# Kernel optimization log

Hardware: AMD Instinct MI355X
Metric: run time of the kernel (lower is better)

Reference implementation:

```python
import jax, jax.numpy as jnp
import numpy as np

B, C, H, W = 8, 128, 64, 64

def conv2d(x, w, b, pad):
    # x: [B,C,H,W], w: [O,I,kh,kw] -> NCHW conv with symmetric padding
    y = jax.lax.conv_general_dilated(
        x, w, window_strides=(1, 1), padding=[(pad, pad), (pad, pad)],
        dimension_numbers=("NCHW", "OIHW", "NCHW"))
    return y + b[None, :, None, None]

def setup_inputs() -> dict:
    key = jax.random.key(0)
    ks = jax.random.split(key, 5)
    s3 = 1.0 / np.sqrt(C * 9)  # kaiming-uniform-ish scale for 3x3 conv
    s1 = 1.0 / np.sqrt(C)
    return {
        "x": jax.random.normal(ks[0], (B, C, H, W), jnp.float32),
        "Wq": jax.random.normal(ks[1], (C, C, 3, 3), jnp.float32) * s3,
        "bq": jnp.zeros((C,), jnp.float32),
        "Wk": jax.random.normal(ks[2], (C, C, 3, 3), jnp.float32) * s3,
        "bk": jnp.zeros((C,), jnp.float32),
        "Wv": jax.random.normal(ks[3], (C, C, 3, 3), jnp.float32) * s3,
        "bv": jnp.zeros((C,), jnp.float32),
        "Wo": jax.random.normal(ks[4], (C, C, 1, 1), jnp.float32) * s1,
        "bo": jnp.zeros((C,), jnp.float32),
    }

def reference(x, Wq, bq, Wk, bk, Wv, bv, Wo, bo):
    b, c, h, w = x.shape
    n = h * w
    scale = c ** (-0.5)
    # NOTE: original module defines self.norm but never applies it in forward.
    q = conv2d(x, Wq, bq, 1).reshape(b, c, n)
    k = conv2d(x, Wk, bk, 1).reshape(b, c, n)
    v = conv2d(x, Wv, bv, 1).reshape(b, c, n)
    attn = jax.nn.softmax(jnp.einsum("bci,bcj->bij", q, k) * scale, axis=2)  # [b,n,n]
    out = jnp.einsum("bij,bcj->bci", attn, v).reshape(b, c, h, w)
    out = conv2d(out, Wo, bo, 0)
    return x + out
```

## Files before the change

kernel.cpp:

```cpp
#include <hip/hip_runtime.h>

typedef __attribute__((ext_vector_type(8))) short bf16x8;
typedef __attribute__((ext_vector_type(4))) float f32x4;
typedef __attribute__((ext_vector_type(16))) float f32x16;

static __device__ __forceinline__ unsigned short f2bf(float f) {
    union { float f; unsigned int u; } v; v.f = f;
    unsigned int r = v.u + 0x7FFFu + ((v.u >> 16) & 1u);
    return (unsigned short)(r >> 16);
}

static __device__ __forceinline__ unsigned cvtpk_bf16(float lo, float hi) {
    unsigned r;
    asm("v_cvt_pk_bf16_f32 %0, %1, %2" : "=v"(r) : "v"(lo), "v"(hi));
    return r;
}

#define NRW (27 * 16384)

__global__ __launch_bounds__(256) void repack_k(const float* __restrict__ Wq, const float* __restrict__ Wk,
                                                const float* __restrict__ Wv, const float* __restrict__ Wo,
                                                unsigned short* __restrict__ RW, unsigned short* __restrict__ WoB) {
    int t = blockIdx.x * 256 + threadIdx.x;
    if (t < NRW) {
        int s = t & 7, o = (t >> 3) & 127, g = (t >> 10) & 3, cc = (t >> 12) & 3, tap = t >> 14;
        int conv = tap / 9, kk = tap % 9, kh = kk / 3, kw = kk % 3;
        int c = cc * 32 + g * 8 + s;
        const float* W = (conv == 0) ? Wq : ((conv == 1) ? Wk : Wv);
        RW[t] = f2bf(W[((o * 128 + c) * 3 + kh) * 3 + kw]);
    } else {
        int u = t - NRW;
        if (u < 16384) WoB[u] = f2bf(Wo[u]);
    }
}

__global__ __launch_bounds__(256) void qkv_conv_k(const float* __restrict__ x, const unsigned short* __restrict__ RW,
                                                  const float* __restrict__ bq, const float* __restrict__ bk,
                                                  const float* __restrict__ bv,
                                                  unsigned short* __restrict__ q_ws, unsigned short* __restrict__ k_ws,
                                                  unsigned short* __restrict__ v_ws) {
    __shared__ unsigned short xs[3 * 66 * 128];
    const int tid = threadIdx.x;
    const int b = blockIdx.x >> 6, h = blockIdx.x & 63;
    for (int i = tid; i < 3 * 66 * 128; i += 256) xs[i] = 0;
    __syncthreads();
    for (int ch = tid; ch < 3 * 128 * 16; ch += 256) {
        int r3 = ch >> 11, rem = ch & 2047, c = rem >> 4, w4 = rem & 15;
        int hh = h - 1 + r3;
        if (hh >= 0 && hh < 64) {
            float4 v = *(const float4*)(x + ((b * 128 + c) * 64 + hh) * 64 + w4 * 4);
            float vv[4] = {v.x, v.y, v.z, v.w};
#pragma unroll
            for (int j = 0; j < 4; ++j) {
                int wr = w4 * 4 + j + 1;
                unsigned int byte = (unsigned int)(((r3 * 66 + wr) * 128 + c) * 2) ^ ((wr & 7) << 4);
                *(unsigned short*)((char*)xs + byte) = f2bf(vv[j]);
            }
        }
    }
    __syncthreads();
    const int lane = tid & 63, wave = tid >> 6;
    const int l15 = lane & 15, g = lane >> 4;
    f32x4 acc[4][6];
#pragma unroll
    for (int i = 0; i < 4; ++i)
#pragma unroll
        for (int j = 0; j < 6; ++j) acc[i][j] = (f32x4){0.f, 0.f, 0.f, 0.f};
#pragma unroll 1
    for (int kk = 0; kk < 9; ++kk) {
        const int kw = kk % 3;
#pragma unroll 1
        for (int cc = 0; cc < 4; ++cc) {
            bf16x8 a[4];
#pragma unroll
            for (int mf = 0; mf < 4; ++mf) {
                int wr = mf * 16 + l15 + kw;
                unsigned int byte = (unsigned int)((((kk / 3) * 66 + wr) * 128 + cc * 32 + g * 8) * 2) ^ ((wr & 7) << 4);
                a[mf] = *(const bf16x8*)((const char*)xs + byte);
            }
#pragma unroll
            for (int n6 = 0; n6 < 6; ++n6) {
                int nt = wave * 6 + n6;
                int conv = nt >> 3;
                int o = (nt * 16 + l15) & 127;
                bf16x8 bfr = *(const bf16x8*)(RW + ((((conv * 9 + kk) * 4 + cc) * 4 + g) * 128 + o) * 8);
#pragma unroll
                for (int mf = 0; mf < 4; ++mf)
                    acc[mf][n6] = __builtin_amdgcn_mfma_f32_16x16x32_bf16(a[mf], bfr, acc[mf][n6], 0, 0, 0);
            }
        }
    }
    const float SCALE = 0.08838834764831845f;
#pragma unroll
    for (int n6 = 0; n6 < 6; ++n6) {
        int nt = wave * 6 + n6;
        int conv = nt >> 3;
        int o = (nt * 16 + l15) & 127;
        float bias = (conv == 0) ? bq[o] : ((conv == 1) ? bk[o] : bv[o]);
#pragma unroll
        for (int mf = 0; mf < 4; ++mf) {
#pragma unroll
            for (int r = 0; r < 4; ++r) {
                int pos = h * 64 + mf * 16 + g * 4 + r;
                float val = acc[mf][n6][r] + bias;
                if (conv == 0)      q_ws[(b * 4096 + pos) * 128 + o] = f2bf(val * SCALE);
                else if (conv == 1) k_ws[(b * 4096 + pos) * 128 + o] = f2bf(val);
                else                v_ws[(b * 128 + o) * 4096 + pos] = f2bf(val);
            }
        }
    }
}

#define AS1C(p) ((const __attribute__((address_space(1))) void*)(p))
#define AS3(p)  ((__attribute__((address_space(3))) void*)(p))

__global__ __launch_bounds__(512, 2) void attn_k(
    const unsigned short* __restrict__ q_ws, const unsigned short* __restrict__ k_ws,
    const unsigned short* __restrict__ v_ws, const unsigned short* __restrict__ WoB,
    const float* __restrict__ bo, const float* __restrict__ x, float* __restrict__ out) {
    __shared__ __align__(16) char smem[133120];

    const int tid = threadIdx.x;
    const int lane = tid & 63, wave = tid >> 6;
    const int wj = wave & 1, wi = wave >> 1;
    const int l31 = lane & 31, h = lane >> 5;
    const int b = blockIdx.x & 7;
    const int ibase = (blockIdx.x >> 3) * 128;
    const int irow = wi * 32 + l31;

    const char* kg[4]; const char* vg[4]; int ldsoff[4];
#pragma unroll
    for (int q = 0; q < 4; ++q) {
        int slot = (wave * 4 + q) * 64 + lane;
        int row = slot >> 4, s = slot & 15;
        int cs = s ^ (row & 15);
        kg[q] = (const char*)(k_ws + ((size_t)b * 4096 + row) * 128 + cs * 8);
        vg[q] = (const char*)(v_ws + ((size_t)b * 128 + row) * 4096 + cs * 8);
        ldsoff[q] = (wave * 4 + q) * 1024;
    }
#pragma unroll
    for (int q = 0; q < 4; ++q)
        __builtin_amdgcn_global_load_lds(AS1C(kg[q]), AS3(smem + ldsoff[q]), 16, 0, 0);
#pragma unroll
    for (int q = 0; q < 4; ++q)
        __builtin_amdgcn_global_load_lds(AS1C(vg[q]), AS3(smem + 32768 + ldsoff[q]), 16, 0, 0);

    bf16x8 qf[8];
    {
        const unsigned short* qrow = q_ws + ((size_t)b * 4096 + ibase + irow) * 128;
#pragma unroll
        for (int cc = 0; cc < 8; ++cc) qf[cc] = *(const bf16x8*)(qrow + cc * 16 + h * 8);
    }

    f32x16 oac[4];
#pragma unroll
    for (int cf = 0; cf < 4; ++cf)
#pragma unroll
        for (int r = 0; r < 16; ++r) oac[cf][r] = 0.f;
    float m = -1e30f, ssum = 0.f;

    __syncthreads();

#pragma unroll 1
    for (int kt = 0; kt < 32; ++kt) {
        const int cur = kt & 1;
        const char* Kc = smem + cur * 65536;
        const char* Vc = Kc + 32768;
        if (kt < 31) {
            char* Kn = smem + (cur ^ 1) * 65536;
            char* Vn = Kn + 32768;
            const size_t kb = (size_t)(kt + 1) * 32768;
            const size_t vb = (size_t)(kt + 1) * 256;
#pragma unroll
            for (int q = 0; q < 4; ++q)
                __builtin_amdgcn_global_load_lds(AS1C(kg[q] + kb), AS3(Kn + ldsoff[q]), 16, 0, 0);
#pragma unroll
            for (int q = 0; q < 4; ++q)
                __builtin_amdgcn_global_load_lds(AS1C(vg[q] + vb), AS3(Vn + ldsoff[q]), 16, 0, 0);
        }

        f32x16 st[2];
#pragma unroll
        for (int jf = 0; jf < 2; ++jf)
#pragma unroll
            for (int r = 0; r < 16; ++r) st[jf][r] = 0.f;
#pragma unroll
        for (int jf = 0; jf < 2; ++jf) {
            const int jrow = wj * 64 + jf * 32 + l31;
#pragma unroll
            for (int cc = 0; cc < 8; ++cc) {
                unsigned byte = (unsigned)(jrow * 256 + cc * 32 + h * 16) ^ ((jrow & 15) << 4);
                bf16x8 kf = *(const bf16x8*)(Kc + byte);
                st[jf] = __builtin_amdgcn_mfma_f32_32x32x16_bf16(kf, qf[cc], st[jf], 0, 0, 0);
            }
        }

        float tmax = -1e30f;
#pragma unroll
        for (int jf = 0; jf < 2; ++jf)
#pragma unroll
            for (int r = 0; r < 16; ++r) tmax = fmaxf(tmax, st[jf][r]);
        tmax = fmaxf(tmax, __shfl_xor(tmax, 32));
        if (!__all(tmax <= m)) {
            float mnew = fmaxf(m, tmax);
            float corr = __expf(m - mnew);
            ssum *= corr;
#pragma unroll
            for (int cf = 0; cf < 4; ++cf)
#pragma unroll
                for (int r = 0; r < 16; ++r) oac[cf][r] *= corr;
            m = mnew;
        }
        float psum = 0.f;
        unsigned u[2][4][2];
#pragma unroll
        for (int jf = 0; jf < 2; ++jf)
#pragma unroll
            for (int gq = 0; gq < 4; ++gq) {
                float p0 = __expf(st[jf][gq * 4 + 0] - m);
                float p1 = __expf(st[jf][gq * 4 + 1] - m);
                float p2 = __expf(st[jf][gq * 4 + 2] - m);
                float p3 = __expf(st[jf][gq * 4 + 3] - m);
                psum += (p0 + p1) + (p2 + p3);
                u[jf][gq][0] = cvtpk_bf16(p0, p1);
                u[jf][gq][1] = cvtpk_bf16(p2, p3);
            }
        psum += __shfl_xor(psum, 32);
        ssum += psum;

        bf16x8 pa[4];
#pragma unroll
        for (int js = 0; js < 4; ++js) {
            const int jf = js >> 1, ga = 2 * (js & 1), gb = ga + 1;
            unsigned own0 = h ? u[jf][gb][0] : u[jf][ga][0];
            unsigned own1 = h ? u[jf][gb][1] : u[jf][ga][1];
            unsigned snd0 = h ? u[jf][ga][0] : u[jf][gb][0];
            unsigned snd1 = h ? u[jf][ga][1] : u[jf][gb][1];
            unsigned rcv0 = __shfl_xor(snd0, 32);
            unsigned rcv1 = __shfl_xor(snd1, 32);
            union { unsigned w[4]; bf16x8 v; } pu;
            pu.w[0] = h ? rcv0 : own0;
            pu.w[1] = h ? rcv1 : own1;
            pu.w[2] = h ? own0 : rcv0;
            pu.w[3] = h ? own1 : rcv1;
            pa[js] = pu.v;
        }

#pragma unroll
        for (int js = 0; js < 4; ++js) {
            const int jcol = wj * 64 + js * 16 + h * 8;
#pragma unroll
            for (int cf = 0; cf < 4; ++cf) {
                int crow = cf * 32 + l31;
                unsigned vbyte = (unsigned)(crow * 256 + jcol * 2) ^ ((crow & 15) << 4);
                bf16x8 va = *(const bf16x8*)(Vc + vbyte);
                oac[cf] = __builtin_amdgcn_mfma_f32_32x32x16_bf16(va, pa[js], oac[cf], 0, 0, 0);
            }
        }
        __syncthreads();
    }

    float* sRed = (float*)(smem + 131072);
    if (h == 0) {
        sRed[(wave * 32 + l31) * 2] = m;
        sRed[(wave * 32 + l31) * 2 + 1] = ssum;
    }
    __syncthreads();
    float m1 = sRed[((wave ^ 1) * 32 + l31) * 2];
    float s1 = sRed[((wave ^ 1) * 32 + l31) * 2 + 1];
    float M = fmaxf(m, m1);
    float aS = __expf(m - M);
    float stot = aS * ssum + __expf(m1 - M) * s1;
    float inv = 1.0f / stot;

    float* sBig = (float*)smem;
    if (wj == 1) {
#pragma unroll
        for (int cf = 0; cf < 4; ++cf)
#pragma unroll
            for (int gq = 0; gq < 4; ++gq) {
                f32x4 v4;
#pragma unroll
                for (int k = 0; k < 4; ++k) v4[k] = aS * oac[cf][gq * 4 + k];
                int cb = cf * 32 + gq * 8 + 4 * h;
                unsigned byte = (unsigned)(wi * 16384 + l31 * 512 + cb * 4) ^ ((l31 & 7) << 4);
                *(f32x4*)((char*)sBig + byte) = v4;
            }
    }
    __syncthreads();
    unsigned short* sOut = (unsigned short*)(smem + 65536);
    if (wj == 0) {
#pragma unroll
        for (int cf = 0; cf < 4; ++cf)
#pragma unroll
            for (int gq = 0; gq < 4; ++gq) {
                int cb = cf * 32 + gq * 8 + 4 * h;
                unsigned rbyte = (unsigned)(wi * 16384 + l31 * 512 + cb * 4) ^ ((l31 & 7) << 4);
                f32x4 o4 = *(const f32x4*)((const char*)sBig + rbyte);
                float t0 = (aS * oac[cf][gq * 4 + 0] + o4[0]) * inv;
                float t1 = (aS * oac[cf][gq * 4 + 1] + o4[1]) * inv;
                float t2 = (aS * oac[cf][gq * 4 + 2] + o4[2]) * inv;
                float t3 = (aS * oac[cf][gq * 4 + 3] + o4[3]) * inv;
                uint2 pk;
                pk.x = cvtpk_bf16(t0, t1);
                pk.y = cvtpk_bf16(t2, t3);
                unsigned wbyte = (unsigned)(irow * 256 + cb * 2) ^ ((irow & 15) << 4);
                *(uint2*)((char*)sOut + wbyte) = pk;
            }
    }
    __syncthreads();

#pragma unroll
    for (int t = 0; t < 2; ++t) {
        int tt = wave + t * 8;
        int of = tt >> 2, ifl = tt & 3;
        int ir = ifl * 32 + l31;
        f32x16 acc;
#pragma unroll
        for (int r = 0; r < 16; ++r) acc[r] = 0.f;
#pragma unroll
        for (int cc = 0; cc < 8; ++cc) {
            unsigned bbyte = (unsigned)(ir * 256 + cc * 32 + h * 16) ^ ((ir & 15) << 4);
            bf16x8 bfr = *(const bf16x8*)((const char*)sOut + bbyte);
            bf16x8 wa = *(const bf16x8*)(WoB + (of * 32 + l31) * 128 + cc * 16 + h * 8);
            acc = __builtin_amdgcn_mfma_f32_32x32x16_bf16(wa, bfr, acc, 0, 0, 0);
        }
        int iglob = ibase + ir;
#pragma unroll
        for (int r = 0; r < 16; ++r) {
            int o = of * 32 + (r & 3) + 8 * (r >> 2) + 4 * h;
            size_t gidx = ((size_t)b * 128 + o) * 4096 + iglob;
            out[gidx] = acc[r] + bo[o] + x[gidx];
        }
    }
}

extern "C" void kernel_launch(void* const* d_in, const int* in_sizes, int n_in,
                              void* d_out, int out_size, void* d_ws, size_t ws_size,
                              hipStream_t stream) {
    const float* x  = (const float*)d_in[0];
    const float* Wq = (const float*)d_in[1];
    const float* bq = (const float*)d_in[2];
    const float* Wk = (const float*)d_in[3];
    const float* bk = (const float*)d_in[4];
    const float* Wv = (const float*)d_in[5];
    const float* bv = (const float*)d_in[6];
    const float* Wo = (const float*)d_in[7];
    const float* bo = (const float*)d_in[8];
    char* ws = (char*)d_ws;
    unsigned short* q_ws = (unsigned short*)(ws);
    unsigned short* k_ws = (unsigned short*)(ws + 8388608);
    unsigned short* v_ws = (unsigned short*)(ws + 16777216);
    unsigned short* RW   = (unsigned short*)(ws + 25165824);
    unsigned short* WoB  = (unsigned short*)(ws + 26050560);
    float* out = (float*)d_out;

    hipLaunchKernelGGL(repack_k, dim3(1792), dim3(256), 0, stream, Wq, Wk, Wv, Wo, RW, WoB);
    hipLaunchKernelGGL(qkv_conv_k, dim3(512), dim3(256), 0, stream, x, RW, bq, bk, bv, q_ws, k_ws, v_ws);
    hipLaunchKernelGGL(attn_k, dim3(256), dim3(512), 0, stream, q_ws, k_ws, v_ws, WoB, bo, x, out);
}
```

Before: 151.4 us.

## Split attention waves 2x4 so each K fragment feeds two query tiles

The attention kernel's wave layout changes from 4 query groups by 2 key splits to 2 query groups by 4 key splits. Each wave now holds two 32-row query tiles, so every K and V fragment read from LDS is reused across two MFMAs, halving LDS read traffic per MFMA. The P transpose now uses permlane32_swap instead of shuffles, and the final merge of the four partial softmax states takes an extra LDS reduction step. Accumulator registers double, which risks spills or lower occupancy. The conv kernel's inner channel loop is also unrolled by two.

```diff
diff --git a/kernel.cpp b/kernel.cpp
--- a/kernel.cpp
+++ b/kernel.cpp
@@ -69,7 +69,7 @@
 #pragma unroll 1
     for (int kk = 0; kk < 9; ++kk) {
         const int kw = kk % 3;
-#pragma unroll 1
+#pragma unroll 2
         for (int cc = 0; cc < 4; ++cc) {
             bf16x8 a[4];
 #pragma unroll
@@ -118,15 +118,14 @@
     const unsigned short* __restrict__ q_ws, const unsigned short* __restrict__ k_ws,
     const unsigned short* __restrict__ v_ws, const unsigned short* __restrict__ WoB,
     const float* __restrict__ bo, const float* __restrict__ x, float* __restrict__ out) {
-    __shared__ __align__(16) char smem[133120];
+    __shared__ __align__(16) char smem[135168];
 
     const int tid = threadIdx.x;
     const int lane = tid & 63, wave = tid >> 6;
-    const int wj = wave & 1, wi = wave >> 1;
+    const int wj = wave & 3, wi = wave >> 2;
     const int l31 = lane & 31, h = lane >> 5;
     const int b = blockIdx.x & 7;
     const int ibase = (blockIdx.x >> 3) * 128;
-    const int irow = wi * 32 + l31;
 
     const char* kg[4]; const char* vg[4]; int ldsoff[4];
 #pragma unroll
@@ -145,19 +144,22 @@
     for (int q = 0; q < 4; ++q)
         __builtin_amdgcn_global_load_lds(AS1C(vg[q]), AS3(smem + 32768 + ldsoff[q]), 16, 0, 0);
 
-    bf16x8 qf[8];
-    {
-        const unsigned short* qrow = q_ws + ((size_t)b * 4096 + ibase + irow) * 128;
-#pragma unroll
-        for (int cc = 0; cc < 8; ++cc) qf[cc] = *(const bf16x8*)(qrow + cc * 16 + h * 8);
-    }
-
-    f32x16 oac[4];
+    bf16x8 qf[2][8];
+#pragma unroll
+    for (int iq = 0; iq < 2; ++iq) {
+        const unsigned short* qrow = q_ws + ((size_t)b * 4096 + ibase + wi * 64 + iq * 32 + l31) * 128;
+#pragma unroll
+        for (int cc = 0; cc < 8; ++cc) qf[iq][cc] = *(const bf16x8*)(qrow + cc * 16 + h * 8);
+    }
+
+    f32x16 oac[4][2];
 #pragma unroll
     for (int cf = 0; cf < 4; ++cf)
 #pragma unroll
-        for (int r = 0; r < 16; ++r) oac[cf][r] = 0.f;
-    float m = -1e30f, ssum = 0.f;
+        for (int iq = 0; iq < 2; ++iq)
+#pragma unroll
+            for (int r = 0; r < 16; ++r) oac[cf][iq][r] = 0.f;
+    float m[2] = {-1e30f, -1e30f}, ssum[2] = {0.f, 0.f};
 
     __syncthreads();
 
@@ -181,80 +183,85 @@
 
         f32x16 st[2];
 #pragma unroll
-        for (int jf = 0; jf < 2; ++jf)
-#pragma unroll
-            for (int r = 0; r < 16; ++r) st[jf][r] = 0.f;
-#pragma unroll
-        for (int jf = 0; jf < 2; ++jf) {
-            const int jrow = wj * 64 + jf * 32 + l31;
-#pragma unroll
-            for (int cc = 0; cc < 8; ++cc) {
-                unsigned byte = (unsigned)(jrow * 256 + cc * 32 + h * 16) ^ ((jrow & 15) << 4);
-                bf16x8 kf = *(const bf16x8*)(Kc + byte);
-                st[jf] = __builtin_amdgcn_mfma_f32_32x32x16_bf16(kf, qf[cc], st[jf], 0, 0, 0);
-            }
-        }
-
-        float tmax = -1e30f;
-#pragma unroll
-        for (int jf = 0; jf < 2; ++jf)
-#pragma unroll
-            for (int r = 0; r < 16; ++r) tmax = fmaxf(tmax, st[jf][r]);
-        tmax = fmaxf(tmax, __shfl_xor(tmax, 32));
-        if (!__all(tmax <= m)) {
-            float mnew = fmaxf(m, tmax);
-            float corr = __expf(m - mnew);
-            ssum *= corr;
-#pragma unroll
-            for (int cf = 0; cf < 4; ++cf)
-#pragma unroll
-                for (int r = 0; r < 16; ++r) oac[cf][r] *= corr;
-            m = mnew;
-        }
-        float psum = 0.f;
+        for (int iq = 0; iq < 2; ++iq)
+#pragma unroll
+            for (int r = 0; r < 16; ++r) st[iq][r] = 0.f;
+        const int jrow = wj * 32 + l31;
+#pragma unroll
+        for (int cc = 0; cc < 8; ++cc) {
+            unsigned byte = (unsigned)(jrow * 256 + cc * 32 + h * 16) ^ ((jrow & 15) << 4);
+            bf16x8 kf = *(const bf16x8*)(Kc + byte);
+            st[0] = __builtin_amdgcn_mfma_f32_32x32x16_bf16(kf, qf[0][cc], st[0], 0, 0, 0);
+            st[1] = __builtin_amdgcn_mfma_f32_32x32x16_bf16(kf, qf[1][cc], st[1], 0, 0, 0);
+        }
+
+        float tm[2];
+#pragma unroll
+        for (int iq = 0; iq < 2; ++iq) {
+            float tmax = st[iq][0];
+#pragma unroll
+            for (int r = 1; r < 16; ++r) tmax = fmaxf(tmax, st[iq][r]);
+            tmax = fmaxf(tmax, __shfl_xor(tmax, 32));
+            tm[iq] = tmax;
+        }
+        if (!__all(tm[0] <= m[0] && tm[1] <= m[1])) {
+#pragma unroll
+            for (int iq = 0; iq < 2; ++iq) {
+                float mnew = fmaxf(m[iq], tm[iq]);
+                float corr = __expf(m[iq] - mnew);
+                ssum[iq] *= corr;
+#pragma unroll
+                for (int cf = 0; cf < 4; ++cf)
+#pragma unroll
+                    for (int r = 0; r < 16; ++r) oac[cf][iq][r] *= corr;
+                m[iq] = mnew;
+            }
+        }
         unsigned u[2][4][2];
 #pragma unroll
-        for (int jf = 0; jf < 2; ++jf)
+        for (int iq = 0; iq < 2; ++iq) {
+            float psum = 0.f;
 #pragma unroll
             for (int gq = 0; gq < 4; ++gq) {
-                float p0 = __expf(st[jf][gq * 4 + 0] - m);
-                float p1 = __expf(st[jf][gq * 4 + 1] - m);
-                float p2 = __expf(st[jf][gq * 4 + 2] - m);
-                float p3 = __expf(st[jf][gq * 4 + 3] - m);
+                float p0 = __expf(st[iq][gq * 4 + 0] - m[iq]);
+                float p1 = __expf(st[iq][gq * 4 + 1] - m[iq]);
+                float p2 = __expf(st[iq][gq * 4 + 2] - m[iq]);
+                float p3 = __expf(st[iq][gq * 4 + 3] - m[iq]);
                 psum += (p0 + p1) + (p2 + p3);
-                u[jf][gq][0] = cvtpk_bf16(p0, p1);
-                u[jf][gq][1] = cvtpk_bf16(p2, p3);
-            }
-        psum += __shfl_xor(psum, 32);
-        ssum += psum;
-
-        bf16x8 pa[4];
-#pragma unroll
-        for (int js = 0; js < 4; ++js) {
-            const int jf = js >> 1, ga = 2 * (js & 1), gb = ga + 1;
-            unsigned own0 = h ? u[jf][gb][0] : u[jf][ga][0];
-            unsigned own1 = h ? u[jf][gb][1] : u[jf][ga][1];
-            unsigned snd0 = h ? u[jf][ga][0] : u[jf][gb][0];
-            unsigned snd1 = h ? u[jf][ga][1] : u[jf][gb][1];
-            unsigned rcv0 = __shfl_xor(snd0, 32);
-            unsigned rcv1 = __shfl_xor(snd1, 32);
-            union { unsigned w[4]; bf16x8 v; } pu;
-            pu.w[0] = h ? rcv0 : own0;
-            pu.w[1] = h ? rcv1 : own1;
-            pu.w[2] = h ? own0 : rcv0;
-            pu.w[3] = h ? own1 : rcv1;
-            pa[js] = pu.v;
-        }
-
-#pragma unroll
-        for (int js = 0; js < 4; ++js) {
-            const int jcol = wj * 64 + js * 16 + h * 8;
+                u[iq][gq][0] = cvtpk_bf16(p0, p1);
+                u[iq][gq][1] = cvtpk_bf16(p2, p3);
+            }
+            psum += __shfl_xor(psum, 32);
+            ssum[iq] += psum;
+        }
+
+        bf16x8 pa[2][2];
+#pragma unroll
+        for (int js = 0; js < 2; ++js)
+#pragma unroll
+            for (int iq = 0; iq < 2; ++iq) {
+                unsigned a0 = u[iq][2 * js][0], b0 = u[iq][2 * js + 1][0];
+                unsigned a1 = u[iq][2 * js][1], b1 = u[iq][2 * js + 1][1];
+                auto r0 = __builtin_amdgcn_permlane32_swap(a0, b0, false, false);
+                auto r1 = __builtin_amdgcn_permlane32_swap(a1, b1, false, false);
+                union { unsigned w[4]; bf16x8 v; } pu;
+                pu.w[0] = r0[0];
+                pu.w[1] = r1[0];
+                pu.w[2] = r0[1];
+                pu.w[3] = r1[1];
+                pa[js][iq] = pu.v;
+            }
+
+#pragma unroll
+        for (int js = 0; js < 2; ++js) {
+            const int jcol = wj * 32 + js * 16 + h * 8;
 #pragma unroll
             for (int cf = 0; cf < 4; ++cf) {
                 int crow = cf * 32 + l31;
                 unsigned vbyte = (unsigned)(crow * 256 + jcol * 2) ^ ((crow & 15) << 4);
                 bf16x8 va = *(const bf16x8*)(Vc + vbyte);
-                oac[cf] = __builtin_amdgcn_mfma_f32_32x32x16_bf16(va, pa[js], oac[cf], 0, 0, 0);
+                oac[cf][0] = __builtin_amdgcn_mfma_f32_32x32x16_bf16(va, pa[js][0], oac[cf][0], 0, 0, 0);
+                oac[cf][1] = __builtin_amdgcn_mfma_f32_32x32x16_bf16(va, pa[js][1], oac[cf][1], 0, 0, 0);
             }
         }
         __syncthreads();
@@ -262,51 +269,101 @@
 
     float* sRed = (float*)(smem + 131072);
     if (h == 0) {
-        sRed[(wave * 32 + l31) * 2] = m;
-        sRed[(wave * 32 + l31) * 2 + 1] = ssum;
-    }
-    __syncthreads();
-    float m1 = sRed[((wave ^ 1) * 32 + l31) * 2];
-    float s1 = sRed[((wave ^ 1) * 32 + l31) * 2 + 1];
-    float M = fmaxf(m, m1);
-    float aS = __expf(m - M);
-    float stot = aS * ssum + __expf(m1 - M) * s1;
-    float inv = 1.0f / stot;
-
-    float* sBig = (float*)smem;
-    if (wj == 1) {
+#pragma unroll
+        for (int iq = 0; iq < 2; ++iq) {
+            int it = wi * 64 + iq * 32 + l31;
+            sRed[(wj * 128 + it) * 2] = m[iq];
+            sRed[(wj * 128 + it) * 2 + 1] = ssum[iq];
+        }
+    }
+    __syncthreads();
+    float aS[2];
+#pragma unroll
+    for (int iq = 0; iq < 2; ++iq) {
+        int it = wi * 64 + iq * 32 + l31;
+        float m0 = sRed[(0 * 128 + it) * 2], s0 = sRed[(0 * 128 + it) * 2 + 1];
+        float m1 = sRed[(1 * 128 + it) * 2], s1 = sRed[(1 * 128 + it) * 2 + 1];
+        float m2 = sRed[(2 * 128 + it) * 2], s2 = sRed[(2 * 128 + it) * 2 + 1];
+        float m3 = sRed[(3 * 128 + it) * 2], s3 = sRed[(3 * 128 + it) * 2 + 1];
+        float M = fmaxf(fmaxf(m0, m1), fmaxf(m2, m3));
+        float stot = __expf(m0 - M) * s0 + __expf(m1 - M) * s1 + __expf(m2 - M) * s2 + __expf(m3 - M) * s3;
+        aS[iq] = __expf(m[iq] - M) / stot;
+    }
+
+    float* sBig0 = (float*)smem;
+    float* sBig1 = (float*)(smem + 65536);
+    if (wj >= 2) {
+        char* B = (wj == 2) ? (char*)sBig0 : (char*)sBig1;
 #pragma unroll
         for (int cf = 0; cf < 4; ++cf)
 #pragma unroll
-            for (int gq = 0; gq < 4; ++gq) {
-                f32x4 v4;
-#pragma unroll
-                for (int k = 0; k < 4; ++k) v4[k] = aS * oac[cf][gq * 4 + k];
-                int cb = cf * 32 + gq * 8 + 4 * h;
-                unsigned byte = (unsigned)(wi * 16384 + l31 * 512 + cb * 4) ^ ((l31 & 7) << 4);
-                *(f32x4*)((char*)sBig + byte) = v4;
-            }
-    }
-    __syncthreads();
-    unsigned short* sOut = (unsigned short*)(smem + 65536);
+            for (int iq = 0; iq < 2; ++iq)
+#pragma unroll
+                for (int g = 0; g < 4; ++g) {
+                    int it = wi * 64 + iq * 32 + l31;
+                    int c = cf * 32 + g * 8 + 4 * h;
+                    f32x4 v;
+#pragma unroll
+                    for (int k = 0; k < 4; ++k) v[k] = oac[cf][iq][4 * g + k] * aS[iq];
+                    unsigned byte = (unsigned)(it * 512 + c * 4) ^ ((it & 7) << 4);
+                    *(f32x4*)(B + byte) = v;
+                }
+    }
+    __syncthreads();
     if (wj == 0) {
 #pragma unroll
         for (int cf = 0; cf < 4; ++cf)
 #pragma unroll
-            for (int gq = 0; gq < 4; ++gq) {
-                int cb = cf * 32 + gq * 8 + 4 * h;
-                unsigned rbyte = (unsigned)(wi * 16384 + l31 * 512 + cb * 4) ^ ((l31 & 7) << 4);
-                f32x4 o4 = *(const f32x4*)((const char*)sBig + rbyte);
-                float t0 = (aS * oac[cf][gq * 4 + 0] + o4[0]) * inv;
-                float t1 = (aS * oac[cf][gq * 4 + 1] + o4[1]) * inv;
-                float t2 = (aS * oac[cf][gq * 4 + 2] + o4[2]) * inv;
-                float t3 = (aS * oac[cf][gq * 4 + 3] + o4[3]) * inv;
-                uint2 pk;
-                pk.x = cvtpk_bf16(t0, t1);
-                pk.y = cvtpk_bf16(t2, t3);
-                unsigned wbyte = (unsigned)(irow * 256 + cb * 2) ^ ((irow & 15) << 4);
-                *(uint2*)((char*)sOut + wbyte) = pk;
-            }
+            for (int iq = 0; iq < 2; ++iq)
+#pragma unroll
+                for (int g = 0; g < 4; ++g) {
+                    int it = wi * 64 + iq * 32 + l31;
+                    int c = cf * 32 + g * 8 + 4 * h;
+                    unsigned byte = (unsigned)(it * 512 + c * 4) ^ ((it & 7) << 4);
+                    f32x4 rd = *(const f32x4*)((const char*)sBig0 + byte);
+#pragma unroll
+                    for (int k = 0; k < 4; ++k) oac[cf][iq][4 * g + k] = oac[cf][iq][4 * g + k] * aS[iq] + rd[k];
+                }
+    } else if (wj == 1) {
+#pragma unroll
+        for (int cf = 0; cf < 4; ++cf)
+#pragma unroll
+            for (int iq = 0; iq < 2; ++iq)
+#pragma unroll
+                for (int g = 0; g < 4; ++g) {
+                    int it = wi * 64 + iq * 32 + l31;
+                    int c = cf * 32 + g * 8 + 4 * h;
+                    unsigned byte = (unsigned)(it * 512 + c * 4) ^ ((it & 7) << 4);
+                    f32x4 rd = *(const f32x4*)((const char*)sBig1 + byte);
+                    f32x4 v;
+#pragma unroll
+                    for (int k = 0; k < 4; ++k) v[k] = oac[cf][iq][4 * g + k] * aS[iq] + rd[k];
+                    *(f32x4*)((char*)sBig1 + byte) = v;
+                }
+    }
+    __syncthreads();
+    unsigned short* sOut = (unsigned short*)smem;
+    if (wj == 0) {
+#pragma unroll
+        for (int cf = 0; cf < 4; ++cf)
+#pragma unroll
+            for (int iq = 0; iq < 2; ++iq)
+#pragma unroll
+                for (int g = 0; g < 4; ++g) {
+                    int it = wi * 64 + iq * 32 + l31;
+                    int c = cf * 32 + g * 8 + 4 * h;
+                    unsigned rbyte = (unsigned)(it * 512 + c * 4) ^ ((it & 7) << 4);
+                    f32x4 r1 = *(const f32x4*)((const char*)sBig1 + rbyte);
+                    float t0 = oac[cf][iq][4 * g + 0] + r1[0];
+                    float t1 = oac[cf][iq][4 * g + 1] + r1[1];
+                    float t2 = oac[cf][iq][4 * g + 2] + r1[2];
+                    float t3 = oac[cf][iq][4 * g + 3] + r1[3];
+                    uint2 pk;
+                    pk.x = cvtpk_bf16(t0, t1);
+                    pk.y = cvtpk_bf16(t2, t3);
+                    unsigned wbyte = (unsigned)(it * 256 + c * 2) ^ ((it & 15) << 4);
+                    *(uint2*)((char*)sOut + wbyte) = pk;
+                }
     }
     __syncthreads();
 
```

Result: slower. 280.0 us (+84.9%).

## Shrink attention tiles to 64 queries and 64 keys, doubling grid

Applied to the files above, without the earlier changes.

The attention kernel now uses 256-thread blocks that each handle 64 query rows, streaming 64-key K/V tiles (previously 128 and 128) with a smaller LDS footprint. The grid doubles to 512 blocks so more CUs stay busy. It also swaps the cross-half P exchange from shuffles to permlane32_swap, adds s_setprio around the MFMA sections, and unrolls the conv channel loop by two. In exchange there are twice as many loop iterations and barriers, K/V traffic per query rises, and each wave holds a smaller score tile.

```diff
diff --git a/kernel.cpp b/kernel.cpp
--- a/kernel.cpp
+++ b/kernel.cpp
@@ -69,7 +69,7 @@
 #pragma unroll 1
     for (int kk = 0; kk < 9; ++kk) {
         const int kw = kk % 3;
-#pragma unroll 1
+#pragma unroll 2
         for (int cc = 0; cc < 4; ++cc) {
             bf16x8 a[4];
 #pragma unroll
@@ -114,40 +114,45 @@
 #define AS1C(p) ((const __attribute__((address_space(1))) void*)(p))
 #define AS3(p)  ((__attribute__((address_space(3))) void*)(p))
 
-__global__ __launch_bounds__(512, 2) void attn_k(
+__global__ __launch_bounds__(256, 2) void attn_k(
     const unsigned short* __restrict__ q_ws, const unsigned short* __restrict__ k_ws,
     const unsigned short* __restrict__ v_ws, const unsigned short* __restrict__ WoB,
     const float* __restrict__ bo, const float* __restrict__ x, float* __restrict__ out) {
-    __shared__ __align__(16) char smem[133120];
+    __shared__ __align__(16) char smem[66560];
 
     const int tid = threadIdx.x;
     const int lane = tid & 63, wave = tid >> 6;
     const int wj = wave & 1, wi = wave >> 1;
     const int l31 = lane & 31, h = lane >> 5;
     const int b = blockIdx.x & 7;
-    const int ibase = (blockIdx.x >> 3) * 128;
-    const int irow = wi * 32 + l31;
-
-    const char* kg[4]; const char* vg[4]; int ldsoff[4];
-#pragma unroll
-    for (int q = 0; q < 4; ++q) {
-        int slot = (wave * 4 + q) * 64 + lane;
-        int row = slot >> 4, s = slot & 15;
-        int cs = s ^ (row & 15);
-        kg[q] = (const char*)(k_ws + ((size_t)b * 4096 + row) * 128 + cs * 8);
-        vg[q] = (const char*)(v_ws + ((size_t)b * 128 + row) * 4096 + cs * 8);
-        ldsoff[q] = (wave * 4 + q) * 1024;
-    }
-#pragma unroll
-    for (int q = 0; q < 4; ++q)
-        __builtin_amdgcn_global_load_lds(AS1C(kg[q]), AS3(smem + ldsoff[q]), 16, 0, 0);
-#pragma unroll
-    for (int q = 0; q < 4; ++q)
-        __builtin_amdgcn_global_load_lds(AS1C(vg[q]), AS3(smem + 32768 + ldsoff[q]), 16, 0, 0);
+    const int qt = blockIdx.x >> 3;
+    const int ibase = qt * 64;
+
+    const char* kB = (const char*)(k_ws + (size_t)b * 4096 * 128);
+    const char* vB = (const char*)(v_ws + (size_t)b * 128 * 4096);
+
+    auto stage = [&](int buf, int kt) {
+        char* Kn = smem + buf * 32768;
+        char* Vn = Kn + 16384;
+#pragma unroll
+        for (int q = 0; q < 4; ++q) {
+            int slot = (wave * 4 + q) * 64 + lane;
+            int krow = slot >> 4, ks = slot & 15;
+            int kcs = ks ^ (krow & 15);
+            __builtin_amdgcn_global_load_lds(AS1C(kB + (size_t)(kt * 64 + krow) * 256 + kcs * 16),
+                                             AS3(Kn + slot * 16), 16, 0, 0);
+            int vrow = slot >> 3, vs = slot & 7;
+            int vcs = vs ^ (vrow & 7);
+            __builtin_amdgcn_global_load_lds(AS1C(vB + (size_t)vrow * 8192 + kt * 128 + vcs * 16),
+                                             AS3(Vn + slot * 16), 16, 0, 0);
+        }
+    };
+
+    stage(0, 0);
 
     bf16x8 qf[8];
     {
-        const unsigned short* qrow = q_ws + ((size_t)b * 4096 + ibase + irow) * 128;
+        const unsigned short* qrow = q_ws + ((size_t)b * 4096 + ibase + wi * 32 + l31) * 128;
 #pragma unroll
         for (int cc = 0; cc < 8; ++cc) qf[cc] = *(const bf16x8*)(qrow + cc * 16 + h * 8);
     }
@@ -162,44 +167,28 @@
     __syncthreads();
 
 #pragma unroll 1
-    for (int kt = 0; kt < 32; ++kt) {
+    for (int kt = 0; kt < 64; ++kt) {
         const int cur = kt & 1;
-        const char* Kc = smem + cur * 65536;
-        const char* Vc = Kc + 32768;
-        if (kt < 31) {
-            char* Kn = smem + (cur ^ 1) * 65536;
-            char* Vn = Kn + 32768;
-            const size_t kb = (size_t)(kt + 1) * 32768;
-            const size_t vb = (size_t)(kt + 1) * 256;
-#pragma unroll
-            for (int q = 0; q < 4; ++q)
-                __builtin_amdgcn_global_load_lds(AS1C(kg[q] + kb), AS3(Kn + ldsoff[q]), 16, 0, 0);
-#pragma unroll
-            for (int q = 0; q < 4; ++q)
-                __builtin_amdgcn_global_load_lds(AS1C(vg[q] + vb), AS3(Vn + ldsoff[q]), 16, 0, 0);
-        }
-
-        f32x16 st[2];
-#pragma unroll
-        for (int jf = 0; jf < 2; ++jf)
-#pragma unroll
-            for (int r = 0; r < 16; ++r) st[jf][r] = 0.f;
-#pragma unroll
-        for (int jf = 0; jf < 2; ++jf) {
-            const int jrow = wj * 64 + jf * 32 + l31;
-#pragma unroll
-            for (int cc = 0; cc < 8; ++cc) {
-                unsigned byte = (unsigned)(jrow * 256 + cc * 32 + h * 16) ^ ((jrow & 15) << 4);
-                bf16x8 kf = *(const bf16x8*)(Kc + byte);
-                st[jf] = __builtin_amdgcn_mfma_f32_32x32x16_bf16(kf, qf[cc], st[jf], 0, 0, 0);
-            }
-        }
-
-        float tmax = -1e30f;
-#pragma unroll
-        for (int jf = 0; jf < 2; ++jf)
-#pragma unroll
-            for (int r = 0; r < 16; ++r) tmax = fmaxf(tmax, st[jf][r]);
+        const char* Kc = smem + cur * 32768;
+        const char* Vc = Kc + 16384;
+        if (kt < 63) stage(cur ^ 1, kt + 1);
+
+        f32x16 st;
+#pragma unroll
+        for (int r = 0; r < 16; ++r) st[r] = 0.f;
+        const int jrow = wj * 32 + l31;
+        __builtin_amdgcn_s_setprio(1);
+#pragma unroll
+        for (int cc = 0; cc < 8; ++cc) {
+            unsigned byte = (unsigned)(jrow * 256 + (((cc * 2 + h) ^ (jrow & 15)) << 4));
+            bf16x8 kf = *(const bf16x8*)(Kc + byte);
+            st = __builtin_amdgcn_mfma_f32_32x32x16_bf16(kf, qf[cc], st, 0, 0, 0);
+        }
+        __builtin_amdgcn_s_setprio(0);
+
+        float tmax = st[0];
+#pragma unroll
+        for (int r = 1; r < 16; ++r) tmax = fmaxf(tmax, st[r]);
         tmax = fmaxf(tmax, __shfl_xor(tmax, 32));
         if (!__all(tmax <= m)) {
             float mnew = fmaxf(m, tmax);
@@ -211,100 +200,95 @@
                 for (int r = 0; r < 16; ++r) oac[cf][r] *= corr;
             m = mnew;
         }
-        float psum = 0.f;
-        unsigned u[2][4][2];
-#pragma unroll
-        for (int jf = 0; jf < 2; ++jf)
-#pragma unroll
-            for (int gq = 0; gq < 4; ++gq) {
-                float p0 = __expf(st[jf][gq * 4 + 0] - m);
-                float p1 = __expf(st[jf][gq * 4 + 1] - m);
-                float p2 = __expf(st[jf][gq * 4 + 2] - m);
-                float p3 = __expf(st[jf][gq * 4 + 3] - m);
-                psum += (p0 + p1) + (p2 + p3);
-                u[jf][gq][0] = cvtpk_bf16(p0, p1);
-                u[jf][gq][1] = cvtpk_bf16(p2, p3);
-            }
-        psum += __shfl_xor(psum, 32);
-        ssum += psum;
-
-        bf16x8 pa[4];
-#pragma unroll
-        for (int js = 0; js < 4; ++js) {
-            const int jf = js >> 1, ga = 2 * (js & 1), gb = ga + 1;
-            unsigned own0 = h ? u[jf][gb][0] : u[jf][ga][0];
-            unsigned own1 = h ? u[jf][gb][1] : u[jf][ga][1];
-            unsigned snd0 = h ? u[jf][ga][0] : u[jf][gb][0];
-            unsigned snd1 = h ? u[jf][ga][1] : u[jf][gb][1];
-            unsigned rcv0 = __shfl_xor(snd0, 32);
-            unsigned rcv1 = __shfl_xor(snd1, 32);
+
+        float ps = 0.f;
+        bf16x8 pa[2];
+#pragma unroll
+        for (int js = 0; js < 2; ++js) {
+            float pA0 = __expf(st[8 * js + 0] - m);
+            float pA1 = __expf(st[8 * js + 1] - m);
+            float pA2 = __expf(st[8 * js + 2] - m);
+            float pA3 = __expf(st[8 * js + 3] - m);
+            float pB0 = __expf(st[8 * js + 4] - m);
+            float pB1 = __expf(st[8 * js + 5] - m);
+            float pB2 = __expf(st[8 * js + 6] - m);
+            float pB3 = __expf(st[8 * js + 7] - m);
+            ps += ((pA0 + pA1) + (pA2 + pA3)) + ((pB0 + pB1) + (pB2 + pB3));
+            unsigned a0 = cvtpk_bf16(pA0, pA1), a1 = cvtpk_bf16(pA2, pA3);
+            unsigned b0 = cvtpk_bf16(pB0, pB1), b1 = cvtpk_bf16(pB2, pB3);
+            auto r0 = __builtin_amdgcn_permlane32_swap(a0, b0, false, false);
+            auto r1 = __builtin_amdgcn_permlane32_swap(a1, b1, false, false);
             union { unsigned w[4]; bf16x8 v; } pu;
-            pu.w[0] = h ? rcv0 : own0;
-            pu.w[1] = h ? rcv1 : own1;
-            pu.w[2] = h ? own0 : rcv0;
-            pu.w[3] = h ? own1 : rcv1;
+            pu.w[0] = r0[0];
+            pu.w[1] = r1[0];
+            pu.w[2] = r0[1];
+            pu.w[3] = r1[1];
             pa[js] = pu.v;
         }
-
-#pragma unroll
-        for (int js = 0; js < 4; ++js) {
-            const int jcol = wj * 64 + js * 16 + h * 8;
+        ps += __shfl_xor(ps, 32);
+        ssum += ps;
+
+        __builtin_amdgcn_s_setprio(1);
+#pragma unroll
+        for (int js = 0; js < 2; ++js) {
+            const int chunk = wj * 4 + js * 2 + h;
 #pragma unroll
             for (int cf = 0; cf < 4; ++cf) {
                 int crow = cf * 32 + l31;
-                unsigned vbyte = (unsigned)(crow * 256 + jcol * 2) ^ ((crow & 15) << 4);
+                unsigned vbyte = (unsigned)(crow * 128 + ((chunk ^ (crow & 7)) << 4));
                 bf16x8 va = *(const bf16x8*)(Vc + vbyte);
                 oac[cf] = __builtin_amdgcn_mfma_f32_32x32x16_bf16(va, pa[js], oac[cf], 0, 0, 0);
             }
         }
+        __builtin_amdgcn_s_setprio(0);
         __syncthreads();
     }
 
-    float* sRed = (float*)(smem + 131072);
+    float* sRed = (float*)(smem + 65536);
+    const int it = wi * 32 + l31;
     if (h == 0) {
-        sRed[(wave * 32 + l31) * 2] = m;
-        sRed[(wave * 32 + l31) * 2 + 1] = ssum;
-    }
-    __syncthreads();
-    float m1 = sRed[((wave ^ 1) * 32 + l31) * 2];
-    float s1 = sRed[((wave ^ 1) * 32 + l31) * 2 + 1];
+        sRed[(wj * 64 + it) * 2] = m;
+        sRed[(wj * 64 + it) * 2 + 1] = ssum;
+    }
+    __syncthreads();
+    float m1 = sRed[((wj ^ 1) * 64 + it) * 2];
+    float s1 = sRed[((wj ^ 1) * 64 + it) * 2 + 1];
     float M = fmaxf(m, m1);
     float aS = __expf(m - M);
-    float stot = aS * ssum + __expf(m1 - M) * s1;
-    float inv = 1.0f / stot;
-
-    float* sBig = (float*)smem;
+    float inv = 1.0f / (aS * ssum + __expf(m1 - M) * s1);
+
+    char* sBig = smem + 32768;
     if (wj == 1) {
 #pragma unroll
         for (int cf = 0; cf < 4; ++cf)
 #pragma unroll
-            for (int gq = 0; gq < 4; ++gq) {
+            for (int g = 0; g < 4; ++g) {
+                int c = cf * 32 + g * 8 + 4 * h;
                 f32x4 v4;
 #pragma unroll
-                for (int k = 0; k < 4; ++k) v4[k] = aS * oac[cf][gq * 4 + k];
-                int cb = cf * 32 + gq * 8 + 4 * h;
-                unsigned byte = (unsigned)(wi * 16384 + l31 * 512 + cb * 4) ^ ((l31 & 7) << 4);
-                *(f32x4*)((char*)sBig + byte) = v4;
-            }
-    }
-    __syncthreads();
-    unsigned short* sOut = (unsigned short*)(smem + 65536);
+                for (int k = 0; k < 4; ++k) v4[k] = aS * oac[cf][4 * g + k];
+                unsigned byte = (unsigned)(it * 512 + c * 4) ^ ((it & 7) << 4);
+                *(f32x4*)(sBig + byte) = v4;
+            }
+    }
+    __syncthreads();
+    unsigned short* sOut = (unsigned short*)smem;
     if (wj == 0) {
 #pragma unroll
         for (int cf = 0; cf < 4; ++cf)
 #pragma unroll
-            for (int gq = 0; gq < 4; ++gq) {
-                int cb = cf * 32 + gq * 8 + 4 * h;
-                unsigned rbyte = (unsigned)(wi * 16384 + l31 * 512 + cb * 4) ^ ((l31 & 7) << 4);
-                f32x4 o4 = *(const f32x4*)((const char*)sBig + rbyte);
-                float t0 = (aS * oac[cf][gq * 4 + 0] + o4[0]) * inv;
-                float t1 = (aS * oac[cf][gq * 4 + 1] + o4[1]) * inv;
-                float t2 = (aS * oac[cf][gq * 4 + 2] + o4[2]) * inv;
-                float t3 = (aS * oac[cf][gq * 4 + 3] + o4[3]) * inv;
+            for (int g = 0; g < 4; ++g) {
+                int c = cf * 32 + g * 8 + 4 * h;
+                unsigned rbyte = (unsigned)(it * 512 + c * 4) ^ ((it & 7) << 4);
+                f32x4 rd = *(const f32x4*)((const char*)sBig + rbyte);
+                float u0 = (aS * oac[cf][4 * g + 0] + rd[0]) * inv;
+                float u1 = (aS * oac[cf][4 * g + 1] + rd[1]) * inv;
+                float u2 = (aS * oac[cf][4 * g + 2] + rd[2]) * inv;
+                float u3 = (aS * oac[cf][4 * g + 3] + rd[3]) * inv;
                 uint2 pk;
-                pk.x = cvtpk_bf16(t0, t1);
-                pk.y = cvtpk_bf16(t2, t3);
-                unsigned wbyte = (unsigned)(irow * 256 + cb * 2) ^ ((irow & 15) << 4);
+                pk.x = cvtpk_bf16(u0, u1);
+                pk.y = cvtpk_bf16(u2, u3);
+                unsigned wbyte = (unsigned)(it * 256 + c * 2) ^ ((it & 15) << 4);
                 *(uint2*)((char*)sOut + wbyte) = pk;
             }
     }
@@ -312,8 +296,8 @@
 
 #pragma unroll
     for (int t = 0; t < 2; ++t) {
-        int tt = wave + t * 8;
-        int of = tt >> 2, ifl = tt & 3;
+        int tt = wave * 2 + t;
+        int of = tt >> 1, ifl = tt & 1;
         int ir = ifl * 32 + l31;
         f32x16 acc;
 #pragma unroll
@@ -357,5 +341,5 @@
 
     hipLaunchKernelGGL(repack_k, dim3(1792), dim3(256), 0, stream, Wq, Wk, Wv, Wo, RW, WoB);
     hipLaunchKernelGGL(qkv_conv_k, dim3(512), dim3(256), 0, stream, x, RW, bq, bk, bv, q_ws, k_ws, v_ws);
-    hipLaunchKernelGGL(attn_k, dim3(256), dim3(512), 0, stream, q_ws, k_ws, v_ws, WoB, bo, x, out);
-}
+    hipLaunchKernelGGL(attn_k, dim3(512), dim3(256), 0, stream, q_ws, k_ws, v_ws, WoB, bo, x, out);
+}
```

New measurement: 162.8 us. +7.5%, slower.
